# Kernel optimization log

Hardware: AMD Instinct MI355X
Metric: run time of the kernel (lower is better)

Reference implementation:

```python
import jax, jax.numpy as jnp
import numpy as np

N_GROUPS = 32
EPS = 1e-6


def group_norm(x, gamma, beta):
    # x: (b, c, h, w); 32 groups, eps=1e-6, affine
    b, c, h, w = x.shape
    xg = x.reshape(b, N_GROUPS, c // N_GROUPS, h, w)
    mean = xg.mean(axis=(2, 3, 4), keepdims=True)
    var = xg.var(axis=(2, 3, 4), keepdims=True)
    xg = (xg - mean) * jax.lax.rsqrt(var + EPS)
    x = xg.reshape(b, c, h, w)
    return x * gamma[None, :, None, None] + beta[None, :, None, None]


def setup_inputs() -> dict:
    key = jax.random.key(0)
    ks = jax.random.split(key, 8)
    b, c, h, w = 4, 512, 64, 64
    sc = 1.0 / np.sqrt(c)
    return {
        "x": jax.random.normal(ks[0], (b, c, h, w), jnp.float32),
        "gn_w": jnp.ones((c,), jnp.float32),
        "gn_b": jnp.zeros((c,), jnp.float32),
        "wq": jax.random.normal(ks[1], (c, c), jnp.float32) * sc,
        "bq": jnp.zeros((c,), jnp.float32),
        "wk": jax.random.normal(ks[2], (c, c), jnp.float32) * sc,
        "bk": jnp.zeros((c,), jnp.float32),
        "wv": jax.random.normal(ks[3], (c, c), jnp.float32) * sc,
        "bv": jnp.zeros((c,), jnp.float32),
        "wo": jax.random.normal(ks[4], (c, c), jnp.float32) * sc,
        "bo": jnp.zeros((c,), jnp.float32),
    }


def reference(x, gn_w, gn_b, wq, bq, wk, bk, wv, bv, wo, bo):
    b, c, h, w = x.shape
    s = c ** (-0.5)
    xn = group_norm(x, gn_w, gn_b)
    xf = xn.reshape(b, c, h * w)  # (b, c, hw)
    # 1x1 convs == channel matmuls: weight (out_c, in_c)
    q = jnp.einsum('oc,bci->boi', wq, xf) + bq[None, :, None]
    k = jnp.einsum('oc,bci->boi', wk, xf) + bk[None, :, None]
    v = jnp.einsum('oc,bci->boi', wv, xf) + bv[None, :, None]
    attn = jnp.einsum('bci,bcj->bij', q, k) * s  # (b, hw, hw)
    attn = jax.nn.softmax(attn, axis=-1)
    out = jnp.einsum('bij,bcj->bci', attn, v)  # (b, c, hw)
    out = jnp.einsum('oc,bci->boi', wo, out) + bo[None, :, None]
    return out.reshape(b, c, h, w) + x
```

## Files before the change

kernel.cpp:

```cpp
#include <hip/hip_runtime.h>

#define B 4
#define C 512
#define HW 4096
#define NG 32
#define GSZ 65536
#define KROW 528

typedef unsigned short u16;
typedef unsigned int u32;
typedef __attribute__((ext_vector_type(8))) short short8;
typedef __attribute__((ext_vector_type(4))) float f32x4;

__device__ __forceinline__ float bf2f(u16 u) {
    union { u32 i; float f; } x; x.i = ((u32)u) << 16; return x.f;
}
__device__ __forceinline__ u16 f2bf(float f) {
    union { u32 i; float f; } x; x.f = f;
    u32 r = x.i + 0x7FFF + ((x.i >> 16) & 1);
    return (u16)(r >> 16);
}
__device__ __forceinline__ u32 cvtpk(float lo, float hi) {
    u32 r;
    asm("v_cvt_pk_bf16_f32 %0, %1, %2" : "=v"(r) : "v"(lo), "v"(hi));
    return r;
}

__device__ __forceinline__ void gld16(const u16* g, u16* l) {
    __builtin_amdgcn_global_load_lds(
        (const __attribute__((address_space(1))) void*)g,
        (__attribute__((address_space(3))) void*)l, 16, 0, 0);
}

__global__ __launch_bounds__(256) void conv_kernel(
        const float* __restrict__ wq, const float* __restrict__ wk,
        const float* __restrict__ wv, const float* __restrict__ wo,
        u16* __restrict__ dst) {
    const int mat = blockIdx.y;
    const float* src = (mat == 0) ? wq : (mat == 1) ? wk : (mat == 2) ? wv : wo;
    const int idx = (blockIdx.x * 256 + threadIdx.x) * 4;
    float4 v = *(const float4*)(src + idx);
    uint2 r = make_uint2(cvtpk(v.x, v.y), cvtpk(v.z, v.w));
    *(uint2*)(dst + (size_t)mat * (C * C) + idx) = r;
}

__global__ __launch_bounds__(256) void gn_stats_kernel(
        const float* __restrict__ x, float2* __restrict__ part) {
    const int gl = blockIdx.x;
    const int qt = blockIdx.y;
    const size_t base = (size_t)gl * GSZ + (size_t)qt * (GSZ / 4);
    const int tid = threadIdx.x;
    float s = 0.f, s2 = 0.f;
    for (int i = tid * 4; i < GSZ / 4; i += 1024) {
        float4 v4 = *(const float4*)(x + base + i);
        s  += v4.x + v4.y + v4.z + v4.w;
        s2 += v4.x*v4.x + v4.y*v4.y + v4.z*v4.z + v4.w*v4.w;
    }
    #pragma unroll
    for (int off = 32; off > 0; off >>= 1) {
        s  += __shfl_down(s, off, 64);
        s2 += __shfl_down(s2, off, 64);
    }
    __shared__ float rs[4], rs2[4];
    int lane = tid & 63, wid = tid >> 6;
    if (lane == 0) { rs[wid] = s; rs2[wid] = s2; }
    __syncthreads();
    if (tid == 0) {
        part[gl * 4 + qt] = make_float2(rs[0] + rs[1] + rs[2] + rs[3],
                                        rs2[0] + rs2[1] + rs2[2] + rs2[3]);
    }
}

__global__ __launch_bounds__(256) void gn_apply_kernel(
        const float* __restrict__ x, const float* __restrict__ gamma,
        const float* __restrict__ beta, const float2* __restrict__ part,
        u16* __restrict__ xnT) {
    const int gl = blockIdx.y;
    const int b = gl >> 5, g = gl & 31;
    const size_t base = (size_t)gl * GSZ;
    const int i0 = blockIdx.x * 512;
    const int tid = threadIdx.x;
    float2 p0 = part[gl * 4 + 0], p1 = part[gl * 4 + 1];
    float2 p2 = part[gl * 4 + 2], p3 = part[gl * 4 + 3];
    float mean = (p0.x + p1.x + p2.x + p3.x) * (1.f / GSZ);
    float var  = (p0.y + p1.y + p2.y + p3.y) * (1.f / GSZ) - mean * mean;
    float rstd = rsqrtf(var + 1e-6f);
    const int c0 = g * 16;
    float gm[16], bt[16];
    #pragma unroll
    for (int c = 0; c < 16; c++) {
        float gg = gamma[c0 + c] * rstd;
        gm[c] = gg;
        bt[c] = beta[c0 + c] - mean * gg;
    }
    #pragma unroll 2
    for (int i = i0 + tid; i < i0 + 512; i += 256) {
        u32 pk[8];
        #pragma unroll
        for (int c = 0; c < 16; c += 2) {
            float a0 = x[base + (size_t)c * HW + i] * gm[c] + bt[c];
            float a1 = x[base + (size_t)(c + 1) * HW + i] * gm[c + 1] + bt[c + 1];
            pk[c >> 1] = cvtpk(a0, a1);
        }
        u16* dst = xnT + ((size_t)b * HW + i) * C + c0;
        *(uint4*)dst       = make_uint4(pk[0], pk[1], pk[2], pk[3]);
        *(uint4*)(dst + 8) = make_uint4(pk[4], pk[5], pk[6], pk[7]);
    }
}

__global__ __launch_bounds__(256) void qkv_kernel(
        const u16* __restrict__ xnT, const u16* __restrict__ wb,
        const float* __restrict__ bq, const float* __restrict__ bk,
        const float* __restrict__ bv,
        u16* __restrict__ qT, u16* __restrict__ kT, u16* __restrict__ vimg) {
    const int mat = blockIdx.y >> 2;
    const int oT0 = (blockIdx.y & 3) * 128;
    const int iT0 = blockIdx.x * 128;
    const int b = blockIdx.z;
    const u16* Ag = xnT + ((size_t)b * HW + iT0) * C;
    const u16* Bg = wb + (size_t)mat * C * C + (size_t)oT0 * C;
    const float* bias = (mat == 0) ? bq : (mat == 1) ? bk : bv;

    const int tid = threadIdx.x;
    const int w = tid >> 6, lane = tid & 63;
    const int qd = lane >> 4, nn = lane & 15;
    const int wm = w & 1, wn = w >> 1;

    __shared__ __align__(16) u16 As[2][128 * 32];
    __shared__ __align__(16) u16 Bs[2][128 * 32];

    f32x4 acc[4][4];
    #pragma unroll
    for (int mt = 0; mt < 4; mt++)
        #pragma unroll
        for (int nt = 0; nt < 4; nt++) acc[mt][nt] = (f32x4){0.f, 0.f, 0.f, 0.f};

    auto stage = [&](u16* dst, const u16* g, int c0) {
        #pragma unroll
        for (int p = 0; p < 2; p++) {
            int rbase = 32 * w + 16 * p;
            int row = rbase + (lane >> 2);
            gld16(g + (size_t)row * C + c0 + (((lane & 3) ^ ((row >> 1) & 3)) << 3),
                  dst + rbase * 32);
        }
    };

    stage(As[0], Ag, 0);
    stage(Bs[0], Bg, 0);

    for (int kt = 0; kt < 16; kt++) {
        const int cur = kt & 1;
        __syncthreads();
        if (kt < 15) {
            stage(As[cur ^ 1], Ag, (kt + 1) * 32);
            stage(Bs[cur ^ 1], Bg, (kt + 1) * 32);
        }
        short8 af[4], bf[4];
        #pragma unroll
        for (int mt = 0; mt < 4; mt++) {
            int row = 64 * wm + 16 * mt + nn;
            af[mt] = *(const short8*)&As[cur][row * 32 + ((qd ^ ((row >> 1) & 3)) << 3)];
        }
        #pragma unroll
        for (int nt = 0; nt < 4; nt++) {
            int row = 64 * wn + 16 * nt + nn;
            bf[nt] = *(const short8*)&Bs[cur][row * 32 + ((qd ^ ((row >> 1) & 3)) << 3)];
        }
        #pragma unroll
        for (int mt = 0; mt < 4; mt++)
            #pragma unroll
            for (int nt = 0; nt < 4; nt++)
                acc[mt][nt] = __builtin_amdgcn_mfma_f32_16x16x32_bf16(af[mt], bf[nt], acc[mt][nt], 0, 0, 0);
    }

    if (mat < 2) {
        u16* dstT = ((mat == 0) ? qT : kT) + (size_t)b * HW * C;
        #pragma unroll
        for (int nt = 0; nt < 4; nt++) {
            int o = oT0 + 64 * wn + 16 * nt + nn;
            float bb = bias[o];
            #pragma unroll
            for (int mt = 0; mt < 4; mt++) {
                int ib = iT0 + 64 * wm + 16 * mt + qd * 4;
                u16* p = dstT + (size_t)ib * C + o;
                p[0]     = f2bf(acc[mt][nt][0] + bb);
                p[C]     = f2bf(acc[mt][nt][1] + bb);
                p[2 * C] = f2bf(acc[mt][nt][2] + bb);
                p[3 * C] = f2bf(acc[mt][nt][3] + bb);
            }
        }
    } else {
        u16* vb = vimg + (size_t)b * 128 * 16384;
        #pragma unroll
        for (int nt = 0; nt < 4; nt++) {
            int c = oT0 + 64 * wn + 16 * nt + nn;
            float bb = bias[c];
            #pragma unroll
            for (int mt = 0; mt < 4; mt++) {
                int ib = iT0 + 64 * wm + 16 * mt + qd * 4;
                int ch = ib >> 5;
                int j0 = ib & 31;
                union { uint2 u; ushort4 s; } st;
                st.u = make_uint2(cvtpk(acc[mt][nt][0] + bb, acc[mt][nt][1] + bb),
                                  cvtpk(acc[mt][nt][2] + bb, acc[mt][nt][3] + bb));
                *(ushort4*)&vb[(size_t)ch * 16384 + c * 32 +
                               (((j0 >> 3) ^ ((c >> 2) & 3)) << 3) + (j0 & 7)] = st.s;
            }
        }
    }
}

__global__ __launch_bounds__(256, 2) void attn_kernel(
        const u16* __restrict__ qT, const u16* __restrict__ kT,
        const u16* __restrict__ vimg, u16* __restrict__ oT) {
    const int b = blockIdx.y;
    const int i0 = blockIdx.x * 32;
    const int tid = threadIdx.x;
    const int w = tid >> 6;
    const int lane = tid & 63;
    const int q = lane >> 4;
    const int n = lane & 15;
    const int rw = w & 1;
    const int jh = w >> 1;

    __shared__ __align__(16) u16 kbuf[2][32 * KROW];
    __shared__ __align__(16) u16 pbuf[2][32 * 40];
    __shared__ __align__(16) float mflag[2][4];
    __shared__ __align__(16) float lpart[2][32];

    short8 qf[16];
    {
        const u16* qrow = qT + ((size_t)b * HW + i0 + rw * 16 + n) * C + q * 8;
        #pragma unroll
        for (int k = 0; k < 16; k++) {
            uint4 u = *(const uint4*)(qrow + k * 32);
            qf[k] = *(const short8*)&u;
        }
    }
    f32x4 oacc[2][8];
    #pragma unroll
    for (int mt = 0; mt < 2; mt++)
        #pragma unroll
        for (int nt = 0; nt < 8; nt++)
            oacc[mt][nt] = (f32x4){0.f, 0.f, 0.f, 0.f};
    float mreg = 0.f;
    float lsum[4] = {0.f, 0.f, 0.f, 0.f};

    const u16* kTb = kT + (size_t)b * HW * C;
    const u16* vTb = vimg + (size_t)b * 128 * 16384;

    auto stageK = [&](int gc, int buf) {
        const u16* gk = kTb + (size_t)gc * 32 * C;
        #pragma unroll
        for (int ii = 0; ii < 8; ii++) {
            int j = w * 8 + ii;
            gld16(gk + (size_t)j * C + ((lane ^ (j & 7)) << 3), &kbuf[buf][j * KROW]);
        }
    };

    const float scale = 0.04419417382415922f;
    stageK(0, 0);
    stageK(1, 1);
    __syncthreads();

    auto s_phase = [&](int slot, int par, float alpha) {
        f32x4 s0 = {0.f,0.f,0.f,0.f}, s1 = {0.f,0.f,0.f,0.f};
        f32x4 s2 = {0.f,0.f,0.f,0.f}, s3 = {0.f,0.f,0.f,0.f};
        const int sw = n & 7;
        const u16* kb = kbuf[slot] + (jh * 16 + n) * KROW;
        __builtin_amdgcn_s_setprio(1);
        #pragma unroll
        for (int m = 0; m < 4; m++) {
            short8 b0 = *(const short8*)&kb[(((4 * m + 0) * 4 + q) ^ sw) << 3];
            short8 b1 = *(const short8*)&kb[(((4 * m + 1) * 4 + q) ^ sw) << 3];
            short8 b2 = *(const short8*)&kb[(((4 * m + 2) * 4 + q) ^ sw) << 3];
            short8 b3 = *(const short8*)&kb[(((4 * m + 3) * 4 + q) ^ sw) << 3];
            s0 = __builtin_amdgcn_mfma_f32_16x16x32_bf16(qf[4 * m + 0], b0, s0, 0, 0, 0);
            s1 = __builtin_amdgcn_mfma_f32_16x16x32_bf16(qf[4 * m + 1], b1, s1, 0, 0, 0);
            s2 = __builtin_amdgcn_mfma_f32_16x16x32_bf16(qf[4 * m + 2], b2, s2, 0, 0, 0);
            s3 = __builtin_amdgcn_mfma_f32_16x16x32_bf16(qf[4 * m + 3], b3, s3, 0, 0, 0);
        }
        __builtin_amdgcn_s_setprio(0);
        float sv[4];
        #pragma unroll
        for (int r = 0; r < 4; r++) sv[r] = ((s0[r] + s1[r]) + (s2[r] + s3[r])) * scale;
        float pm = fmaxf(fmaxf(sv[0], sv[1]), fmaxf(sv[2], sv[3]));
        float flagv = -1e30f;
        if (__any(pm > mreg + 8.0f)) {
            float mx = pm;
            mx = fmaxf(mx, __shfl_xor(mx, 1));
            mx = fmaxf(mx, __shfl_xor(mx, 2));
            mx = fmaxf(mx, __shfl_xor(mx, 4));
            mx = fmaxf(mx, __shfl_xor(mx, 8));
            mx = fmaxf(mx, __shfl_xor(mx, 16));
            mx = fmaxf(mx, __shfl_xor(mx, 32));
            flagv = mx;
        }
        if (lane == 0) mflag[par][w] = flagv;
        float p0 = __expf(sv[0] - mreg), p1 = __expf(sv[1] - mreg);
        float p2 = __expf(sv[2] - mreg), p3 = __expf(sv[3] - mreg);
        lsum[0] = lsum[0] * alpha + p0;
        lsum[1] = lsum[1] * alpha + p1;
        lsum[2] = lsum[2] * alpha + p2;
        lsum[3] = lsum[3] * alpha + p3;
        u32 a = cvtpk(p0, p1), c = cvtpk(p2, p3);
        u16* pb = &pbuf[par][(rw * 16 + q * 4) * 40 + jh * 16 + n];
        pb[0]      = (u16)a;
        pb[40]     = (u16)(a >> 16);
        pb[80]     = (u16)c;
        pb[120]    = (u16)(c >> 16);
    };

    s_phase(0, 0, 1.f);
    __syncthreads();

    #pragma unroll 1
    for (int t = 0; t < 128; ++t) {
        const int cur = t & 1;
        f32x4 fl = *(const f32x4*)mflag[cur];
        short8 pf[2];
        #pragma unroll
        for (int mt = 0; mt < 2; mt++)
            pf[mt] = *(const short8*)&pbuf[cur][(mt * 16 + n) * 40 + q * 8];
        uint4 vpf[8];
        {
            const u16* gv = vTb + (size_t)t * 16384;
            #pragma unroll
            for (int nt = 0; nt < 8; nt++) {
                int c = w * 128 + nt * 16 + n;
                vpf[nt] = *(const uint4*)&gv[c * 32 + ((q ^ ((c >> 2) & 3)) << 3)];
            }
        }
        if (t < 126) stageK(t + 2, cur);
        float mnew = fmaxf(fmaxf(mreg, fl[0]), fmaxf(fmaxf(fl[1], fl[2]), fl[3]));
        float alpha = 1.f;
        if (mnew > mreg) { alpha = __expf(mreg - mnew); mreg = mnew; }
        if (t < 127) {
            s_phase(cur ^ 1, cur ^ 1, alpha);
        } else {
            #pragma unroll
            for (int r = 0; r < 4; r++) lsum[r] *= alpha;
        }
        __builtin_amdgcn_s_setprio(1);
        #pragma unroll
        for (int nt = 0; nt < 8; nt++) {
            short8 vf = *(const short8*)&vpf[nt];
            #pragma unroll
            for (int mt = 0; mt < 2; mt++)
                oacc[mt][nt] = __builtin_amdgcn_mfma_f32_16x16x32_bf16(pf[mt], vf, oacc[mt][nt], 0, 0, 0);
        }
        __builtin_amdgcn_s_setprio(0);
        if (alpha != 1.f) {
            #pragma unroll
            for (int mt = 0; mt < 2; mt++)
                #pragma unroll
                for (int nt = 0; nt < 8; nt++) {
                    oacc[mt][nt][0] *= alpha; oacc[mt][nt][1] *= alpha;
                    oacc[mt][nt][2] *= alpha; oacc[mt][nt][3] *= alpha;
                }
        }
        __syncthreads();
    }
    #pragma unroll
    for (int r = 0; r < 4; r++) {
        float l = lsum[r];
        l += __shfl_xor(l, 1);
        l += __shfl_xor(l, 2);
        l += __shfl_xor(l, 4);
        l += __shfl_xor(l, 8);
        if (n == 0) lpart[jh][rw * 16 + q * 4 + r] = l;
    }
    __syncthreads();
    #pragma unroll
    for (int mt = 0; mt < 2; mt++) {
        float inv[4];
        #pragma unroll
        for (int r = 0; r < 4; r++) {
            int row = mt * 16 + q * 4 + r;
            inv[r] = 1.f / (lpart[0][row] + lpart[1][row]);
        }
        #pragma unroll
        for (int nt = 0; nt < 8; nt++) {
            int cc = w * 128 + nt * 16 + n;
            size_t base = ((size_t)b * HW + i0 + mt * 16 + q * 4) * C + cc;
            oT[base        ] = f2bf(oacc[mt][nt][0] * inv[0]);
            oT[base +   C  ] = f2bf(oacc[mt][nt][1] * inv[1]);
            oT[base + 2 * C] = f2bf(oacc[mt][nt][2] * inv[2]);
            oT[base + 3 * C] = f2bf(oacc[mt][nt][3] * inv[3]);
        }
    }
}

__global__ __launch_bounds__(256) void proj_kernel(
        const u16* __restrict__ oT, const u16* __restrict__ wob,
        const float* __restrict__ bo, const float* __restrict__ x,
        float* __restrict__ out) {
    const int o0 = blockIdx.y * 128;
    const int i0t = blockIdx.x * 128;
    const int b = blockIdx.z;
    const u16* Ag = wob + (size_t)o0 * C;
    const u16* Bg = oT + ((size_t)b * HW + i0t) * C;

    const int tid = threadIdx.x;
    const int w = tid >> 6, lane = tid & 63;
    const int qd = lane >> 4, nn = lane & 15;
    const int wm = w & 1, wn = w >> 1;

    __shared__ __align__(16) u16 As[2][128 * 32];
    __shared__ __align__(16) u16 Bs[2][128 * 32];

    f32x4 acc[4][4];
    #pragma unroll
    for (int mt = 0; mt < 4; mt++)
        #pragma unroll
        for (int nt = 0; nt < 4; nt++) acc[mt][nt] = (f32x4){0.f, 0.f, 0.f, 0.f};

    auto stage = [&](u16* dst, const u16* g, int c0) {
        #pragma unroll
        for (int p = 0; p < 2; p++) {
            int rbase = 32 * w + 16 * p;
            int row = rbase + (lane >> 2);
            gld16(g + (size_t)row * C + c0 + (((lane & 3) ^ ((row >> 1) & 3)) << 3),
                  dst + rbase * 32);
        }
    };

    stage(As[0], Ag, 0);
    stage(Bs[0], Bg, 0);

    for (int kt = 0; kt < 16; kt++) {
        const int cur = kt & 1;
        __syncthreads();
        if (kt < 15) {
            stage(As[cur ^ 1], Ag, (kt + 1) * 32);
            stage(Bs[cur ^ 1], Bg, (kt + 1) * 32);
        }
        short8 af[4], bf[4];
        #pragma unroll
        for (int mt = 0; mt < 4; mt++) {
            int row = 64 * wm + 16 * mt + nn;
            af[mt] = *(const short8*)&As[cur][row * 32 + ((qd ^ ((row >> 1) & 3)) << 3)];
        }
        #pragma unroll
        for (int nt = 0; nt < 4; nt++) {
            int row = 64 * wn + 16 * nt + nn;
            bf[nt] = *(const short8*)&Bs[cur][row * 32 + ((qd ^ ((row >> 1) & 3)) << 3)];
        }
        #pragma unroll
        for (int mt = 0; mt < 4; mt++)
            #pragma unroll
            for (int nt = 0; nt < 4; nt++)
                acc[mt][nt] = __builtin_amdgcn_mfma_f32_16x16x32_bf16(af[mt], bf[nt], acc[mt][nt], 0, 0, 0);
    }

    #pragma unroll
    for (int mt = 0; mt < 4; mt++) {
        #pragma unroll
        for (int r = 0; r < 4; r++) {
            int o = o0 + 64 * wm + 16 * mt + qd * 4 + r;
            float bb = bo[o];
            #pragma unroll
            for (int nt = 0; nt < 4; nt++) {
                int i = i0t + 64 * wn + 16 * nt + nn;
                size_t idx = ((size_t)b * C + o) * HW + i;
                out[idx] = acc[mt][nt][r] + bb + x[idx];
            }
        }
    }
}

extern "C" void kernel_launch(void* const* d_in, const int* in_sizes, int n_in,
                              void* d_out, int out_size, void* d_ws, size_t ws_size,
                              hipStream_t stream) {
    const float* x    = (const float*)d_in[0];
    const float* gn_w = (const float*)d_in[1];
    const float* gn_b = (const float*)d_in[2];
    const float* wq   = (const float*)d_in[3];
    const float* bq   = (const float*)d_in[4];
    const float* wk   = (const float*)d_in[5];
    const float* bk   = (const float*)d_in[6];
    const float* wv   = (const float*)d_in[7];
    const float* bv   = (const float*)d_in[8];
    const float* wo   = (const float*)d_in[9];
    const float* bo   = (const float*)d_in[10];
    float* out = (float*)d_out;

    const size_t WSZ = (size_t)C * C;
    const size_t S1  = (size_t)B * C * HW;
    u16* wb    = (u16*)d_ws;
    u16* wob   = wb + 3 * WSZ;
    u16* xnT   = wob + WSZ;
    u16* qT    = xnT + S1;
    u16* kT    = qT + S1;
    u16* vimg  = kT + S1;
    u16* oT    = vimg + S1;
    float2* part = (float2*)(oT + S1);

    hipLaunchKernelGGL(conv_kernel,     dim3(256, 4), dim3(256), 0, stream, wq, wk, wv, wo, wb);
    hipLaunchKernelGGL(gn_stats_kernel, dim3(B*NG, 4), dim3(256), 0, stream, x, part);
    hipLaunchKernelGGL(gn_apply_kernel, dim3(HW/512, B*NG), dim3(256), 0, stream,
                       x, gn_w, gn_b, part, xnT);
    hipLaunchKernelGGL(qkv_kernel,      dim3(HW/128, 12, B), dim3(256), 0, stream,
                       xnT, wb, bq, bk, bv, qT, kT, vimg);
    hipLaunchKernelGGL(attn_kernel,     dim3(HW/32, B), dim3(256), 0, stream,
                       qT, kT, vimg, oT);
    hipLaunchKernelGGL(proj_kernel,     dim3(HW/128, C/128, B), dim3(256), 0, stream, oT, wob, bo, x, out);
}
```

Measured before the change: 383.7 us.

## Restructure attention to keep Q in LDS and stream K from a chunked global layout

```diff
diff --git a/kernel.cpp b/kernel.cpp
--- a/kernel.cpp
+++ b/kernel.cpp
@@ -5,7 +5,6 @@
 #define HW 4096
 #define NG 32
 #define GSZ 65536
-#define KROW 528
 
 typedef unsigned short u16;
 typedef unsigned int u32;
@@ -112,7 +111,7 @@
         const u16* __restrict__ xnT, const u16* __restrict__ wb,
         const float* __restrict__ bq, const float* __restrict__ bk,
         const float* __restrict__ bv,
-        u16* __restrict__ qT, u16* __restrict__ kT, u16* __restrict__ vimg) {
+        u16* __restrict__ qT, u16* __restrict__ kimg, u16* __restrict__ vimg) {
     const int mat = blockIdx.y >> 2;
     const int oT0 = (blockIdx.y & 3) * 128;
     const int iT0 = blockIdx.x * 128;
@@ -173,8 +172,8 @@
                 acc[mt][nt] = __builtin_amdgcn_mfma_f32_16x16x32_bf16(af[mt], bf[nt], acc[mt][nt], 0, 0, 0);
     }
 
-    if (mat < 2) {
-        u16* dstT = ((mat == 0) ? qT : kT) + (size_t)b * HW * C;
+    if (mat == 0) {
+        u16* dstT = qT + (size_t)b * HW * C;
         #pragma unroll
         for (int nt = 0; nt < 4; nt++) {
             int o = oT0 + 64 * wn + 16 * nt + nn;
@@ -187,6 +186,22 @@
                 p[C]     = f2bf(acc[mt][nt][1] + bb);
                 p[2 * C] = f2bf(acc[mt][nt][2] + bb);
                 p[3 * C] = f2bf(acc[mt][nt][3] + bb);
+            }
+        }
+    } else if (mat == 1) {
+        u16* kb = kimg + (size_t)b * HW * C;
+        #pragma unroll
+        for (int nt = 0; nt < 4; nt++) {
+            int o = oT0 + 64 * wn + 16 * nt + nn;
+            float bb = bias[o];
+            #pragma unroll
+            for (int mt = 0; mt < 4; mt++) {
+                int ib = iT0 + 64 * wm + 16 * mt + qd * 4;
+                u16* p = kb + ((size_t)(o >> 5) * HW + ib) * 32 + (o & 31);
+                p[0]      = f2bf(acc[mt][nt][0] + bb);
+                p[32]     = f2bf(acc[mt][nt][1] + bb);
+                p[64]     = f2bf(acc[mt][nt][2] + bb);
+                p[96]     = f2bf(acc[mt][nt][3] + bb);
             }
         }
     } else {
@@ -211,7 +226,7 @@
 }
 
 __global__ __launch_bounds__(256, 2) void attn_kernel(
-        const u16* __restrict__ qT, const u16* __restrict__ kT,
+        const u16* __restrict__ qT, const u16* __restrict__ kimg,
         const u16* __restrict__ vimg, u16* __restrict__ oT) {
     const int b = blockIdx.y;
     const int i0 = blockIdx.x * 32;
@@ -220,71 +235,75 @@
     const int lane = tid & 63;
     const int q = lane >> 4;
     const int n = lane & 15;
-    const int rw = w & 1;
-    const int jh = w >> 1;
-
-    __shared__ __align__(16) u16 kbuf[2][32 * KROW];
-    __shared__ __align__(16) u16 pbuf[2][32 * 40];
+
+    __shared__ __align__(16) u16 qbuf[32 * 512];
+    __shared__ __align__(16) u16 pbuf[2][32 * 72];
     __shared__ __align__(16) float mflag[2][4];
-    __shared__ __align__(16) float lpart[2][32];
-
-    short8 qf[16];
-    {
-        const u16* qrow = qT + ((size_t)b * HW + i0 + rw * 16 + n) * C + q * 8;
-        #pragma unroll
-        for (int k = 0; k < 16; k++) {
-            uint4 u = *(const uint4*)(qrow + k * 32);
-            qf[k] = *(const short8*)&u;
-        }
-    }
+    __shared__ __align__(16) float lpart[4][32];
+
+    #pragma unroll
+    for (int ii = 0; ii < 8; ii++) {
+        int j = w * 8 + ii;
+        const u16* gq = qT + ((size_t)b * HW + i0 + j) * C;
+        gld16(gq + ((lane ^ (j & 7)) << 3), &qbuf[j * 512]);
+    }
+
     f32x4 oacc[2][8];
     #pragma unroll
     for (int mt = 0; mt < 2; mt++)
         #pragma unroll
-        for (int nt = 0; nt < 8; nt++)
-            oacc[mt][nt] = (f32x4){0.f, 0.f, 0.f, 0.f};
+        for (int ct = 0; ct < 8; ct++)
+            oacc[mt][ct] = (f32x4){0.f, 0.f, 0.f, 0.f};
     float mreg = 0.f;
-    float lsum[4] = {0.f, 0.f, 0.f, 0.f};
-
-    const u16* kTb = kT + (size_t)b * HW * C;
+    float lsum[8] = {0.f,0.f,0.f,0.f,0.f,0.f,0.f,0.f};
+
+    const u16* kbg = kimg + (size_t)b * HW * C;
     const u16* vTb = vimg + (size_t)b * 128 * 16384;
-
-    auto stageK = [&](int gc, int buf) {
-        const u16* gk = kTb + (size_t)gc * 32 * C;
-        #pragma unroll
-        for (int ii = 0; ii < 8; ii++) {
-            int j = w * 8 + ii;
-            gld16(gk + (size_t)j * C + ((lane ^ (j & 7)) << 3), &kbuf[buf][j * KROW]);
-        }
-    };
-
     const float scale = 0.04419417382415922f;
-    stageK(0, 0);
-    stageK(1, 1);
-    __syncthreads();
-
-    auto s_phase = [&](int slot, int par, float alpha) {
-        f32x4 s0 = {0.f,0.f,0.f,0.f}, s1 = {0.f,0.f,0.f,0.f};
-        f32x4 s2 = {0.f,0.f,0.f,0.f}, s3 = {0.f,0.f,0.f,0.f};
-        const int sw = n & 7;
-        const u16* kb = kbuf[slot] + (jh * 16 + n) * KROW;
+
+    auto s_phase = [&](int tc, int par, float alpha) {
+        f32x4 s[2][4];
+        #pragma unroll
+        for (int mt = 0; mt < 2; mt++)
+            #pragma unroll
+            for (int i = 0; i < 4; i++) s[mt][i] = (f32x4){0.f, 0.f, 0.f, 0.f};
+        const int jcol = tc * 64 + w * 16 + n;
+        short8 kf[2][4];
+        #pragma unroll
+        for (int i = 0; i < 4; i++) {
+            uint4 u = *(const uint4*)&kbg[((size_t)i * HW + jcol) * 32 + q * 8];
+            kf[0][i] = *(const short8*)&u;
+        }
+        const int pc0 = n & 7;
         __builtin_amdgcn_s_setprio(1);
         #pragma unroll
-        for (int m = 0; m < 4; m++) {
-            short8 b0 = *(const short8*)&kb[(((4 * m + 0) * 4 + q) ^ sw) << 3];
-            short8 b1 = *(const short8*)&kb[(((4 * m + 1) * 4 + q) ^ sw) << 3];
-            short8 b2 = *(const short8*)&kb[(((4 * m + 2) * 4 + q) ^ sw) << 3];
-            short8 b3 = *(const short8*)&kb[(((4 * m + 3) * 4 + q) ^ sw) << 3];
-            s0 = __builtin_amdgcn_mfma_f32_16x16x32_bf16(qf[4 * m + 0], b0, s0, 0, 0, 0);
-            s1 = __builtin_amdgcn_mfma_f32_16x16x32_bf16(qf[4 * m + 1], b1, s1, 0, 0, 0);
-            s2 = __builtin_amdgcn_mfma_f32_16x16x32_bf16(qf[4 * m + 2], b2, s2, 0, 0, 0);
-            s3 = __builtin_amdgcn_mfma_f32_16x16x32_bf16(qf[4 * m + 3], b3, s3, 0, 0, 0);
+        for (int g = 0; g < 4; g++) {
+            if (g < 3) {
+                #pragma unroll
+                for (int i = 0; i < 4; i++) {
+                    uint4 u = *(const uint4*)&kbg[((size_t)((g + 1) * 4 + i) * HW + jcol) * 32 + q * 8];
+                    kf[(g + 1) & 1][i] = *(const short8*)&u;
+                }
+            }
+            #pragma unroll
+            for (int i = 0; i < 4; i++) {
+                int kw = g * 4 + i;
+                int pc = (((kw * 4 + q) ^ pc0) << 3);
+                short8 a0 = *(const short8*)&qbuf[n * 512 + pc];
+                short8 a1 = *(const short8*)&qbuf[(16 + n) * 512 + pc];
+                s[0][i] = __builtin_amdgcn_mfma_f32_16x16x32_bf16(a0, kf[g & 1][i], s[0][i], 0, 0, 0);
+                s[1][i] = __builtin_amdgcn_mfma_f32_16x16x32_bf16(a1, kf[g & 1][i], s[1][i], 0, 0, 0);
+            }
         }
         __builtin_amdgcn_s_setprio(0);
-        float sv[4];
-        #pragma unroll
-        for (int r = 0; r < 4; r++) sv[r] = ((s0[r] + s1[r]) + (s2[r] + s3[r])) * scale;
-        float pm = fmaxf(fmaxf(sv[0], sv[1]), fmaxf(sv[2], sv[3]));
+        float sv[2][4];
+        #pragma unroll
+        for (int mt = 0; mt < 2; mt++)
+            #pragma unroll
+            for (int r = 0; r < 4; r++)
+                sv[mt][r] = ((s[mt][0][r] + s[mt][1][r]) + (s[mt][2][r] + s[mt][3][r])) * scale;
+        float pm = fmaxf(fmaxf(fmaxf(sv[0][0], sv[0][1]), fmaxf(sv[0][2], sv[0][3])),
+                         fmaxf(fmaxf(sv[1][0], sv[1][1]), fmaxf(sv[1][2], sv[1][3])));
         float flagv = -1e30f;
         if (__any(pm > mreg + 8.0f)) {
             float mx = pm;
@@ -297,79 +316,94 @@
             flagv = mx;
         }
         if (lane == 0) mflag[par][w] = flagv;
-        float p0 = __expf(sv[0] - mreg), p1 = __expf(sv[1] - mreg);
-        float p2 = __expf(sv[2] - mreg), p3 = __expf(sv[3] - mreg);
-        lsum[0] = lsum[0] * alpha + p0;
-        lsum[1] = lsum[1] * alpha + p1;
-        lsum[2] = lsum[2] * alpha + p2;
-        lsum[3] = lsum[3] * alpha + p3;
-        u32 a = cvtpk(p0, p1), c = cvtpk(p2, p3);
-        u16* pb = &pbuf[par][(rw * 16 + q * 4) * 40 + jh * 16 + n];
-        pb[0]      = (u16)a;
-        pb[40]     = (u16)(a >> 16);
-        pb[80]     = (u16)c;
-        pb[120]    = (u16)(c >> 16);
+        float p[2][4];
+        #pragma unroll
+        for (int mt = 0; mt < 2; mt++)
+            #pragma unroll
+            for (int r = 0; r < 4; r++) {
+                p[mt][r] = __expf(sv[mt][r] - mreg);
+                lsum[mt * 4 + r] = lsum[mt * 4 + r] * alpha + p[mt][r];
+            }
+        #pragma unroll
+        for (int mt = 0; mt < 2; mt++) {
+            u32 a = cvtpk(p[mt][0], p[mt][1]);
+            u32 c = cvtpk(p[mt][2], p[mt][3]);
+            u16* pb = &pbuf[par][(mt * 16 + q * 4) * 72 + w * 16 + n];
+            pb[0]       = (u16)a;
+            pb[72]      = (u16)(a >> 16);
+            pb[144]     = (u16)c;
+            pb[216]     = (u16)(c >> 16);
+        }
     };
 
+    __syncthreads();
     s_phase(0, 0, 1.f);
     __syncthreads();
 
     #pragma unroll 1
-    for (int t = 0; t < 128; ++t) {
+    for (int t = 0; t < 64; ++t) {
         const int cur = t & 1;
+        uint4 vf[8][2];
+        {
+            const u16* gv = vTb + ((size_t)2 * t) * 16384;
+            #pragma unroll
+            for (int ct = 0; ct < 8; ct++) {
+                int c = w * 128 + ct * 16 + n;
+                const u16* p0 = gv + c * 32 + ((q ^ ((c >> 2) & 3)) << 3);
+                vf[ct][0] = *(const uint4*)p0;
+                vf[ct][1] = *(const uint4*)(p0 + 16384);
+            }
+        }
         f32x4 fl = *(const f32x4*)mflag[cur];
-        short8 pf[2];
+        short8 pf[2][2];
         #pragma unroll
         for (int mt = 0; mt < 2; mt++)
-            pf[mt] = *(const short8*)&pbuf[cur][(mt * 16 + n) * 40 + q * 8];
-        uint4 vpf[8];
-        {
-            const u16* gv = vTb + (size_t)t * 16384;
-            #pragma unroll
-            for (int nt = 0; nt < 8; nt++) {
-                int c = w * 128 + nt * 16 + n;
-                vpf[nt] = *(const uint4*)&gv[c * 32 + ((q ^ ((c >> 2) & 3)) << 3)];
-            }
-        }
-        if (t < 126) stageK(t + 2, cur);
+            #pragma unroll
+            for (int jw = 0; jw < 2; jw++)
+                pf[mt][jw] = *(const short8*)&pbuf[cur][(mt * 16 + n) * 72 + jw * 32 + q * 8];
         float mnew = fmaxf(fmaxf(mreg, fl[0]), fmaxf(fmaxf(fl[1], fl[2]), fl[3]));
         float alpha = 1.f;
         if (mnew > mreg) { alpha = __expf(mreg - mnew); mreg = mnew; }
-        if (t < 127) {
-            s_phase(cur ^ 1, cur ^ 1, alpha);
-        } else {
-            #pragma unroll
-            for (int r = 0; r < 4; r++) lsum[r] *= alpha;
-        }
         __builtin_amdgcn_s_setprio(1);
         #pragma unroll
-        for (int nt = 0; nt < 8; nt++) {
-            short8 vf = *(const short8*)&vpf[nt];
-            #pragma unroll
-            for (int mt = 0; mt < 2; mt++)
-                oacc[mt][nt] = __builtin_amdgcn_mfma_f32_16x16x32_bf16(pf[mt], vf, oacc[mt][nt], 0, 0, 0);
+        for (int ct = 0; ct < 8; ct++) {
+            #pragma unroll
+            for (int mt = 0; mt < 2; mt++) {
+                oacc[mt][ct] = __builtin_amdgcn_mfma_f32_16x16x32_bf16(
+                    pf[mt][0], *(const short8*)&vf[ct][0], oacc[mt][ct], 0, 0, 0);
+                oacc[mt][ct] = __builtin_amdgcn_mfma_f32_16x16x32_bf16(
+                    pf[mt][1], *(const short8*)&vf[ct][1], oacc[mt][ct], 0, 0, 0);
+            }
         }
         __builtin_amdgcn_s_setprio(0);
         if (alpha != 1.f) {
             #pragma unroll
             for (int mt = 0; mt < 2; mt++)
                 #pragma unroll
-                for (int nt = 0; nt < 8; nt++) {
-                    oacc[mt][nt][0] *= alpha; oacc[mt][nt][1] *= alpha;
-                    oacc[mt][nt][2] *= alpha; oacc[mt][nt][3] *= alpha;
+                for (int ct = 0; ct < 8; ct++) {
+                    oacc[mt][ct][0] *= alpha; oacc[mt][ct][1] *= alpha;
+                    oacc[mt][ct][2] *= alpha; oacc[mt][ct][3] *= alpha;
                 }
         }
+        if (t < 63) {
+            s_phase(t + 1, cur ^ 1, alpha);
+        } else {
+            #pragma unroll
+            for (int r = 0; r < 8; r++) lsum[r] *= alpha;
+        }
         __syncthreads();
     }
     #pragma unroll
-    for (int r = 0; r < 4; r++) {
-        float l = lsum[r];
-        l += __shfl_xor(l, 1);
-        l += __shfl_xor(l, 2);
-        l += __shfl_xor(l, 4);
-        l += __shfl_xor(l, 8);
-        if (n == 0) lpart[jh][rw * 16 + q * 4 + r] = l;
-    }
+    for (int mt = 0; mt < 2; mt++)
+        #pragma unroll
+        for (int r = 0; r < 4; r++) {
+            float l = lsum[mt * 4 + r];
+            l += __shfl_xor(l, 1);
+            l += __shfl_xor(l, 2);
+            l += __shfl_xor(l, 4);
+            l += __shfl_xor(l, 8);
+            if (n == 0) lpart[w][mt * 16 + q * 4 + r] = l;
+        }
     __syncthreads();
     #pragma unroll
     for (int mt = 0; mt < 2; mt++) {
@@ -377,16 +411,16 @@
         #pragma unroll
         for (int r = 0; r < 4; r++) {
             int row = mt * 16 + q * 4 + r;
-            inv[r] = 1.f / (lpart[0][row] + lpart[1][row]);
-        }
-        #pragma unroll
-        for (int nt = 0; nt < 8; nt++) {
-            int cc = w * 128 + nt * 16 + n;
+            inv[r] = 1.f / (lpart[0][row] + lpart[1][row] + lpart[2][row] + lpart[3][row]);
+        }
+        #pragma unroll
+        for (int ct = 0; ct < 8; ct++) {
+            int cc = w * 128 + ct * 16 + n;
             size_t base = ((size_t)b * HW + i0 + mt * 16 + q * 4) * C + cc;
-            oT[base        ] = f2bf(oacc[mt][nt][0] * inv[0]);
-            oT[base +   C  ] = f2bf(oacc[mt][nt][1] * inv[1]);
-            oT[base + 2 * C] = f2bf(oacc[mt][nt][2] * inv[2]);
-            oT[base + 3 * C] = f2bf(oacc[mt][nt][3] * inv[3]);
+            oT[base        ] = f2bf(oacc[mt][ct][0] * inv[0]);
+            oT[base +   C  ] = f2bf(oacc[mt][ct][1] * inv[1]);
+            oT[base + 2 * C] = f2bf(oacc[mt][ct][2] * inv[2]);
+            oT[base + 3 * C] = f2bf(oacc[mt][ct][3] * inv[3]);
         }
     }
 }
@@ -491,8 +525,8 @@
     u16* wob   = wb + 3 * WSZ;
     u16* xnT   = wob + WSZ;
     u16* qT    = xnT + S1;
-    u16* kT    = qT + S1;
-    u16* vimg  = kT + S1;
+    u16* kimg  = qT + S1;
+    u16* vimg  = kimg + S1;
     u16* oT    = vimg + S1;
     float2* part = (float2*)(oT + S1);
 
@@ -501,8 +535,8 @@
     hipLaunchKernelGGL(gn_apply_kernel, dim3(HW/512, B*NG), dim3(256), 0, stream,
                        x, gn_w, gn_b, part, xnT);
     hipLaunchKernelGGL(qkv_kernel,      dim3(HW/128, 12, B), dim3(256), 0, stream,
-                       xnT, wb, bq, bk, bv, qT, kT, vimg);
+                       xnT, wb, bq, bk, bv, qT, kimg, vimg);
     hipLaunchKernelGGL(attn_kernel,     dim3(HW/32, B), dim3(256), 0, stream,
-                       qT, kT, vimg, oT);
+                       qT, kimg, vimg, oT);
     hipLaunchKernelGGL(proj_kernel,     dim3(HW/128, C/128, B), dim3(256), 0, stream, oT, wob, bo, x, out);
 }
```

Measured after the change: 427.2 us. 1.11x slower.

## Stage GN-apply and QKV epilogue stores through LDS for coalesced writes

Applied to the files above, without the earlier changes.

```diff
diff --git a/kernel.cpp b/kernel.cpp
--- a/kernel.cpp
+++ b/kernel.cpp
@@ -75,36 +75,41 @@
         const float* __restrict__ x, const float* __restrict__ gamma,
         const float* __restrict__ beta, const float2* __restrict__ part,
         u16* __restrict__ xnT) {
-    const int gl = blockIdx.y;
-    const int b = gl >> 5, g = gl & 31;
-    const size_t base = (size_t)gl * GSZ;
-    const int i0 = blockIdx.x * 512;
+    const int b = blockIdx.y;
+    const int i0 = blockIdx.x * 32;
     const int tid = threadIdx.x;
-    float2 p0 = part[gl * 4 + 0], p1 = part[gl * 4 + 1];
-    float2 p2 = part[gl * 4 + 2], p3 = part[gl * 4 + 3];
-    float mean = (p0.x + p1.x + p2.x + p3.x) * (1.f / GSZ);
-    float var  = (p0.y + p1.y + p2.y + p3.y) * (1.f / GSZ) - mean * mean;
-    float rstd = rsqrtf(var + 1e-6f);
-    const int c0 = g * 16;
-    float gm[16], bt[16];
-    #pragma unroll
-    for (int c = 0; c < 16; c++) {
-        float gg = gamma[c0 + c] * rstd;
+    __shared__ float gm[512], bt[512];
+    __shared__ __align__(16) u16 tile[32 * 512];
+
+    for (int c = tid; c < 512; c += 256) {
+        int g = c >> 4;
+        const float2* pp = part + ((size_t)b * 32 + g) * 4;
+        float2 p0 = pp[0], p1 = pp[1], p2 = pp[2], p3 = pp[3];
+        float mean = (p0.x + p1.x + p2.x + p3.x) * (1.f / GSZ);
+        float var  = (p0.y + p1.y + p2.y + p3.y) * (1.f / GSZ) - mean * mean;
+        float rstd = rsqrtf(var + 1e-6f);
+        float gg = gamma[c] * rstd;
         gm[c] = gg;
-        bt[c] = beta[c0 + c] - mean * gg;
-    }
-    #pragma unroll 2
-    for (int i = i0 + tid; i < i0 + 512; i += 256) {
-        u32 pk[8];
-        #pragma unroll
-        for (int c = 0; c < 16; c += 2) {
-            float a0 = x[base + (size_t)c * HW + i] * gm[c] + bt[c];
-            float a1 = x[base + (size_t)(c + 1) * HW + i] * gm[c + 1] + bt[c + 1];
-            pk[c >> 1] = cvtpk(a0, a1);
-        }
-        u16* dst = xnT + ((size_t)b * HW + i) * C + c0;
-        *(uint4*)dst       = make_uint4(pk[0], pk[1], pk[2], pk[3]);
-        *(uint4*)(dst + 8) = make_uint4(pk[4], pk[5], pk[6], pk[7]);
+        bt[c] = beta[c] - mean * gg;
+    }
+    __syncthreads();
+    const int ci = tid >> 5;
+    const int ii = tid & 31;
+    const float* xb = x + (size_t)b * 512 * 4096 + i0;
+    #pragma unroll 4
+    for (int p = 0; p < 64; p++) {
+        int c = p * 8 + ci;
+        float v = xb[(size_t)c * 4096 + ii] * gm[c] + bt[c];
+        tile[ii * 512 + (c ^ ((ii & 7) << 3))] = f2bf(v);
+    }
+    __syncthreads();
+    u16* dst = xnT + ((size_t)b * HW + i0) * C;
+    #pragma unroll
+    for (int p = 0; p < 8; p++) {
+        int i = p * 4 + (tid >> 6);
+        int ch = tid & 63;
+        *(uint4*)(dst + (size_t)i * C + ch * 8) =
+            *(const uint4*)&tile[i * 512 + ((ch ^ (i & 7)) << 3)];
     }
 }
 
@@ -126,8 +131,9 @@
     const int qd = lane >> 4, nn = lane & 15;
     const int wm = w & 1, wn = w >> 1;
 
-    __shared__ __align__(16) u16 As[2][128 * 32];
-    __shared__ __align__(16) u16 Bs[2][128 * 32];
+    __shared__ __align__(16) u16 smem[16384];
+    u16* As0 = smem;
+    u16* Bs0 = smem + 8192;
 
     f32x4 acc[4][4];
     #pragma unroll
@@ -145,26 +151,28 @@
         }
     };
 
-    stage(As[0], Ag, 0);
-    stage(Bs[0], Bg, 0);
+    stage(As0, Ag, 0);
+    stage(Bs0, Bg, 0);
 
     for (int kt = 0; kt < 16; kt++) {
         const int cur = kt & 1;
         __syncthreads();
         if (kt < 15) {
-            stage(As[cur ^ 1], Ag, (kt + 1) * 32);
-            stage(Bs[cur ^ 1], Bg, (kt + 1) * 32);
-        }
+            stage(As0 + (cur ^ 1) * 4096, Ag, (kt + 1) * 32);
+            stage(Bs0 + (cur ^ 1) * 4096, Bg, (kt + 1) * 32);
+        }
+        const u16* Ac = As0 + cur * 4096;
+        const u16* Bc = Bs0 + cur * 4096;
         short8 af[4], bf[4];
         #pragma unroll
         for (int mt = 0; mt < 4; mt++) {
             int row = 64 * wm + 16 * mt + nn;
-            af[mt] = *(const short8*)&As[cur][row * 32 + ((qd ^ ((row >> 1) & 3)) << 3)];
+            af[mt] = *(const short8*)&Ac[row * 32 + ((qd ^ ((row >> 1) & 3)) << 3)];
         }
         #pragma unroll
         for (int nt = 0; nt < 4; nt++) {
             int row = 64 * wn + 16 * nt + nn;
-            bf[nt] = *(const short8*)&Bs[cur][row * 32 + ((qd ^ ((row >> 1) & 3)) << 3)];
+            bf[nt] = *(const short8*)&Bc[row * 32 + ((qd ^ ((row >> 1) & 3)) << 3)];
         }
         #pragma unroll
         for (int mt = 0; mt < 4; mt++)
@@ -173,39 +181,56 @@
                 acc[mt][nt] = __builtin_amdgcn_mfma_f32_16x16x32_bf16(af[mt], bf[nt], acc[mt][nt], 0, 0, 0);
     }
 
+    __syncthreads();
+    u16* dt = smem;
+
     if (mat < 2) {
-        u16* dstT = ((mat == 0) ? qT : kT) + (size_t)b * HW * C;
         #pragma unroll
         for (int nt = 0; nt < 4; nt++) {
-            int o = oT0 + 64 * wn + 16 * nt + nn;
-            float bb = bias[o];
+            int o_l = 64 * wn + 16 * nt + nn;
+            float bb = bias[oT0 + o_l];
             #pragma unroll
             for (int mt = 0; mt < 4; mt++) {
-                int ib = iT0 + 64 * wm + 16 * mt + qd * 4;
-                u16* p = dstT + (size_t)ib * C + o;
-                p[0]     = f2bf(acc[mt][nt][0] + bb);
-                p[C]     = f2bf(acc[mt][nt][1] + bb);
-                p[2 * C] = f2bf(acc[mt][nt][2] + bb);
-                p[3 * C] = f2bf(acc[mt][nt][3] + bb);
+                int i_l = 64 * wm + 16 * mt + qd * 4;
+                dt[(i_l + 0) * 128 + o_l] = f2bf(acc[mt][nt][0] + bb);
+                dt[(i_l + 1) * 128 + o_l] = f2bf(acc[mt][nt][1] + bb);
+                dt[(i_l + 2) * 128 + o_l] = f2bf(acc[mt][nt][2] + bb);
+                dt[(i_l + 3) * 128 + o_l] = f2bf(acc[mt][nt][3] + bb);
             }
         }
+        __syncthreads();
+        u16* dstT = ((mat == 0) ? qT : kT) + ((size_t)b * HW + iT0) * C + oT0;
+        #pragma unroll
+        for (int p = 0; p < 8; p++) {
+            int i_l = p * 16 + (tid >> 4);
+            int ch = tid & 15;
+            *(uint4*)(dstT + (size_t)i_l * C + ch * 8) = *(const uint4*)&dt[i_l * 128 + ch * 8];
+        }
     } else {
-        u16* vb = vimg + (size_t)b * 128 * 16384;
         #pragma unroll
         for (int nt = 0; nt < 4; nt++) {
-            int c = oT0 + 64 * wn + 16 * nt + nn;
-            float bb = bias[c];
+            int c_l = 64 * wn + 16 * nt + nn;
+            float bb = bias[oT0 + c_l];
             #pragma unroll
             for (int mt = 0; mt < 4; mt++) {
-                int ib = iT0 + 64 * wm + 16 * mt + qd * 4;
-                int ch = ib >> 5;
-                int j0 = ib & 31;
+                int i_l = 64 * wm + 16 * mt + qd * 4;
+                int lc = i_l >> 5;
+                int j0 = i_l & 31;
                 union { uint2 u; ushort4 s; } st;
                 st.u = make_uint2(cvtpk(acc[mt][nt][0] + bb, acc[mt][nt][1] + bb),
                                   cvtpk(acc[mt][nt][2] + bb, acc[mt][nt][3] + bb));
-                *(ushort4*)&vb[(size_t)ch * 16384 + c * 32 +
-                               (((j0 >> 3) ^ ((c >> 2) & 3)) << 3) + (j0 & 7)] = st.s;
+                *(ushort4*)&dt[lc * 4096 + c_l * 32 +
+                               (((j0 >> 3) ^ ((c_l >> 2) & 3)) << 3) + (j0 & 7)] = st.s;
             }
+        }
+        __syncthreads();
+        u16* vb = vimg + (size_t)b * 128 * 16384;
+        const int chb = iT0 >> 5;
+        #pragma unroll
+        for (int p = 0; p < 8; p++) {
+            int lc = p >> 1, half = p & 1;
+            *(uint4*)(vb + (size_t)(chb + lc) * 16384 + oT0 * 32 + half * 2048 + tid * 8) =
+                *(const uint4*)&dt[lc * 4096 + half * 2048 + tid * 8];
         }
     }
 }
@@ -498,7 +523,7 @@
 
     hipLaunchKernelGGL(conv_kernel,     dim3(256, 4), dim3(256), 0, stream, wq, wk, wv, wo, wb);
     hipLaunchKernelGGL(gn_stats_kernel, dim3(B*NG, 4), dim3(256), 0, stream, x, part);
-    hipLaunchKernelGGL(gn_apply_kernel, dim3(HW/512, B*NG), dim3(256), 0, stream,
+    hipLaunchKernelGGL(gn_apply_kernel, dim3(HW/32, B), dim3(256), 0, stream,
                        x, gn_w, gn_b, part, xnT);
     hipLaunchKernelGGL(qkv_kernel,      dim3(HW/128, 12, B), dim3(256), 0, stream,
                        xnT, wb, bq, bk, bv, qT, kT, vimg);
```

Result: no change. 386.1 us (+0.6%).
